# Performance work log

Measured on AMD Instinct MI355X. Metric: run time of the kernel, lower is better.

Reference implementation:

```python
import jax, jax.numpy as jnp
import numpy as np

EPS = 1e-07
B, N, L, K = 256, 512, 4, 1

def setup_inputs() -> dict:
    key = jax.random.key(0)
    k1, k2, k3, k4 = jax.random.split(key, 4)
    x = jax.random.randint(k1, (B, N), 0, L)
    W = jax.random.normal(k2, (N, N), dtype=jnp.float32)
    V_compress = jax.random.normal(k3, (N, L), dtype=jnp.float32)
    E_compress = jax.random.normal(k4, (K, N, N, L, L), dtype=jnp.float32)
    return {"x": x, "W": W, "V_compress": V_compress, "E_compress": E_compress}

def reference(x, W, V_compress, E_compress):
    n = W.shape[0]
    # V: per-variable marginals via softmax over classes
    V = jax.nn.softmax(V_compress, axis=1)                      # (n, l)
    # E: pairwise joints for mixture 0, normalized over (l, l)
    E = jnp.exp(E_compress[0])                                   # (n, n, l, l)
    E = E / E.sum(axis=(-2, -1), keepdims=True)
    A_b = V[:, None, :, None]                                    # row target marginals
    B_b = V[None, :, None, :]                                    # col target marginals
    # IPFP: 2 iterations of row/col marginal rescaling
    for _ in range(2):
        E = E * (A_b / E.sum(axis=3, keepdims=True))
        E = E * (B_b / E.sum(axis=2, keepdims=True))
        E = E / E.sum(axis=(-2, -1), keepdims=True)
    # zero the diagonal blocks and clamp
    E_mask = (1.0 - jnp.eye(n, dtype=E.dtype))[:, :, None, None]
    E = jnp.clip(E * E_mask, 0.0, 1.0)
    # symmetric edge-weight matrix from W
    Ws = jax.nn.sigmoid(W)
    Ws = jnp.tril(Ws, -1)
    Ws = Ws.T + Ws
    L_0 = -Ws + jnp.diag(Ws.sum(axis=1))                         # (n, n)
    # gather per-sample marginals and pairwise joints
    idx = jnp.arange(n)
    Pr = V[idx[None, :], x]                                      # (B, n): Pr[b,i] = V[i, x[b,i]]
    P = E[idx[:, None], idx[None, :], x[:, :, None], x[:, None, :]]  # (B, n, n)
    P = P / (Pr[:, :, None] * Pr[:, None, :])
    WP = Ws[None, :, :] * P                                      # (B, n, n)
    Lap = -WP + jnp.eye(n, dtype=WP.dtype)[None] * WP.sum(axis=2)[:, :, None]
    # matrix-tree: logdet of the (n-1)x(n-1) minor
    _, ld = jnp.linalg.slogdet(Lap[:, 1:, 1:] + EPS)
    _, ld0 = jnp.linalg.slogdet(L_0[1:, 1:] + EPS)
    y = jnp.log(Pr + EPS).sum(axis=1) + ld - ld0                 # (B,)
    return y
```

## Files before the change

### kernel.cpp

```cpp
#include <hip/hip_runtime.h>

#define NN 512
#define NR 511
#define NB 64
#define BATCH 256
#define NMAT 257
#define EPSF 1e-7f

__device__ __forceinline__ float block_reduce_sum_512(float v, float* red) {
#pragma unroll
  for (int off = 32; off > 0; off >>= 1) v += __shfl_down(v, off, 64);
  int tid = threadIdx.x;
  if ((tid & 63) == 0) red[tid >> 6] = v;
  __syncthreads();
  float s = 0.f;
#pragma unroll
  for (int w = 0; w < 8; ++w) s += red[w];
  return s;
}

__global__ void k_softmaxV(const float* __restrict__ Vc, float* __restrict__ V) {
  int i = threadIdx.x;
  float v0 = Vc[i * 4 + 0], v1 = Vc[i * 4 + 1], v2 = Vc[i * 4 + 2], v3 = Vc[i * 4 + 3];
  float mx = fmaxf(fmaxf(v0, v1), fmaxf(v2, v3));
  float e0 = expf(v0 - mx), e1 = expf(v1 - mx), e2 = expf(v2 - mx), e3 = expf(v3 - mx);
  float s = e0 + e1 + e2 + e3;
  V[i * 4 + 0] = e0 / s; V[i * 4 + 1] = e1 / s; V[i * 4 + 2] = e2 / s; V[i * 4 + 3] = e3 / s;
}

__global__ void k_Ws(const float* __restrict__ W, float* __restrict__ Ws) {
  int i = blockIdx.x, j = threadIdx.x;
  float v = 0.f;
  if (i != j) {
    int hi = i > j ? i : j, lo = i > j ? j : i;
    float wv = W[hi * NN + lo];
    v = 1.f / (1.f + expf(-wv));
  }
  Ws[i * NN + j] = v;
}

__global__ void k_E(const float* __restrict__ Ec, const float* __restrict__ V,
                    float* __restrict__ E) {
  int idx = blockIdx.x * blockDim.x + threadIdx.x;
  if (idx >= NN * NN) return;
  int i = idx >> 9, j = idx & 511;
  float e[16];
  const float* src = Ec + (size_t)idx * 16;
#pragma unroll
  for (int t = 0; t < 16; ++t) e[t] = expf(src[t]);
  float tot = 0.f;
#pragma unroll
  for (int t = 0; t < 16; ++t) tot += e[t];
  float rt = 1.f / tot;
#pragma unroll
  for (int t = 0; t < 16; ++t) e[t] *= rt;
  float Vi[4], Vj[4];
#pragma unroll
  for (int a = 0; a < 4; ++a) { Vi[a] = V[i * 4 + a]; Vj[a] = V[j * 4 + a]; }
#pragma unroll
  for (int it = 0; it < 2; ++it) {
#pragma unroll
    for (int a = 0; a < 4; ++a) {
      float rs = e[a * 4 + 0] + e[a * 4 + 1] + e[a * 4 + 2] + e[a * 4 + 3];
      float sc = Vi[a] / rs;
#pragma unroll
      for (int b = 0; b < 4; ++b) e[a * 4 + b] *= sc;
    }
#pragma unroll
    for (int b = 0; b < 4; ++b) {
      float cs = e[0 + b] + e[4 + b] + e[8 + b] + e[12 + b];
      float sc = Vj[b] / cs;
#pragma unroll
      for (int a = 0; a < 4; ++a) e[a * 4 + b] *= sc;
    }
    float t2 = 0.f;
#pragma unroll
    for (int t = 0; t < 16; ++t) t2 += e[t];
    float rt2 = 1.f / t2;
#pragma unroll
    for (int t = 0; t < 16; ++t) e[t] *= rt2;
  }
  float* dst = E + (size_t)idx * 16;
  bool diag = (i == j);
#pragma unroll
  for (int t = 0; t < 16; ++t) {
    float v = diag ? 0.f : e[t];
    dst[t] = fminf(fmaxf(v, 0.f), 1.f);
  }
}

__global__ __launch_bounds__(512)
void k_Pr(const int* __restrict__ x, const float* __restrict__ V,
          float* __restrict__ rPr, float* __restrict__ logPr) {
  __shared__ float red[8];
  int b = blockIdx.x, i = threadIdx.x;
  int xi = x[b * NN + i];
  float pr = V[i * 4 + xi];
  rPr[b * NN + i] = 1.f / pr;
  float s = block_reduce_sum_512(logf(pr + EPSF), red);
  if (i == 0) logPr[b] = s;
}

__global__ __launch_bounds__(512)
void k_build(const int* __restrict__ x, const float* __restrict__ Ws,
             const float* __restrict__ E, const float* __restrict__ rPr,
             float* __restrict__ mats, int m0) {
  int slot = blockIdx.y;
  int m = m0 + slot;
  float* A = mats + (size_t)slot * NN * NN;
  int wv = threadIdx.x >> 6, lane = threadIdx.x & 63;
  int r = blockIdx.x * 8 + wv;
  float* dst = A + (size_t)r * NN + lane * 8;
  if (r == NR) {
    float4 z0 = {0.f, 0.f, 0.f, 0.f};
    float4 z1 = {0.f, 0.f, 0.f, 0.f};
    if (lane == 63) z1.w = 1.f;
    *(float4*)dst = z0;
    *(float4*)(dst + 4) = z1;
    return;
  }
  int i = r + 1;
  int j0 = lane * 8;
  float4 wsa = *(const float4*)&Ws[i * NN + j0];
  float4 wsb = *(const float4*)&Ws[i * NN + j0 + 4];
  float wp[8];
  if (m < BATCH) {
    const int* xm = x + (size_t)m * NN;
    int xi = xm[i];
    int4 xa = *(const int4*)&xm[j0];
    int4 xb = *(const int4*)&xm[j0 + 4];
    const float* rp = rPr + (size_t)m * NN;
    float rpi = rp[i];
    float4 ra = *(const float4*)&rp[j0];
    float4 rb = *(const float4*)&rp[j0 + 4];
    const float* Eb = E + ((((size_t)i << 9) + j0) << 4) + (xi << 2);
    wp[0] = wsa.x * Eb[0 * 16 + xa.x] * (rpi * ra.x);
    wp[1] = wsa.y * Eb[1 * 16 + xa.y] * (rpi * ra.y);
    wp[2] = wsa.z * Eb[2 * 16 + xa.z] * (rpi * ra.z);
    wp[3] = wsa.w * Eb[3 * 16 + xa.w] * (rpi * ra.w);
    wp[4] = wsb.x * Eb[4 * 16 + xb.x] * (rpi * rb.x);
    wp[5] = wsb.y * Eb[5 * 16 + xb.y] * (rpi * rb.y);
    wp[6] = wsb.z * Eb[6 * 16 + xb.z] * (rpi * rb.z);
    wp[7] = wsb.w * Eb[7 * 16 + xb.w] * (rpi * rb.w);
  } else {
    wp[0] = wsa.x; wp[1] = wsa.y; wp[2] = wsa.z; wp[3] = wsa.w;
    wp[4] = wsb.x; wp[5] = wsb.y; wp[6] = wsb.z; wp[7] = wsb.w;
  }
  float rs = ((wp[0] + wp[1]) + (wp[2] + wp[3])) + ((wp[4] + wp[5]) + (wp[6] + wp[7]));
#pragma unroll
  for (int o = 32; o > 0; o >>= 1) rs += __shfl_xor(rs, o, 64);
  float nxt = __shfl_down(wp[0], 1, 64);
  float sh[8] = {wp[1], wp[2], wp[3], wp[4], wp[5], wp[6], wp[7], nxt};
  float out[8];
#pragma unroll
  for (int t = 0; t < 8; ++t) {
    int c = j0 + t;
    float v = -sh[t] + EPSF;
    if (c == r) v += rs;
    if (c == NR) v = 0.f;
    out[t] = v;
  }
  float4 o0 = {out[0], out[1], out[2], out[3]};
  float4 o1 = {out[4], out[5], out[6], out[7]};
  *(float4*)dst = o0;
  *(float4*)(dst + 4) = o1;
}

template <int S>
struct PStepF {
  static __device__ __forceinline__ void run(float (&rr)[64], float (*Prow)[64],
                                             bool own, int tid, float& lgsum) {
    float rinv = 1.f / Prow[S & 1][S];
    if (own && tid > S) {
      float l = rr[S] * rinv;
      rr[S] = l;
      constexpr int C0 = S + 1;
      constexpr int A4 = (C0 + 3) & ~3;
#pragma unroll
      for (int c = C0; c < (A4 < 64 ? A4 : 64); ++c)
        rr[c] = fmaf(-l, Prow[S & 1][c], rr[c]);
#pragma unroll
      for (int g = A4 / 4; g < 16; ++g) {
        float4 u = *(const float4*)&Prow[S & 1][g * 4];
        rr[g * 4 + 0] = fmaf(-l, u.x, rr[g * 4 + 0]);
        rr[g * 4 + 1] = fmaf(-l, u.y, rr[g * 4 + 1]);
        rr[g * 4 + 2] = fmaf(-l, u.z, rr[g * 4 + 2]);
        rr[g * 4 + 3] = fmaf(-l, u.w, rr[g * 4 + 3]);
      }
    }
    if (S + 1 < 64) {
      if (tid == S + 1) {
        lgsum += logf(rr[S + 1]);
#pragma unroll
        for (int c4 = (S + 1) >> 2; c4 < 16; ++c4) {
          float4 v = {rr[c4 * 4 + 0], rr[c4 * 4 + 1], rr[c4 * 4 + 2], rr[c4 * 4 + 3]};
          *(float4*)&Prow[(S + 1) & 1][c4 * 4] = v;
        }
      }
    }
    __syncthreads();
    PStepF<S + 1>::run(rr, Prow, own, tid, lgsum);
  }
};
template <>
struct PStepF<64> {
  static __device__ __forceinline__ void run(float (&)[64], float (*)[64],
                                             bool, int, float&) {}
};

template <int Q>
struct UStep {
  static __device__ __forceinline__ void run(float (&a)[64], const float* L) {
    constexpr int j0 = Q * 4;
    a[j0 + 1] = fmaf(-L[(j0 + 1) * 68 + j0], a[j0], a[j0 + 1]);
    a[j0 + 2] = fmaf(-L[(j0 + 2) * 68 + j0], a[j0], a[j0 + 2]);
    a[j0 + 2] = fmaf(-L[(j0 + 2) * 68 + j0 + 1], a[j0 + 1], a[j0 + 2]);
    a[j0 + 3] = fmaf(-L[(j0 + 3) * 68 + j0], a[j0], a[j0 + 3]);
    a[j0 + 3] = fmaf(-L[(j0 + 3) * 68 + j0 + 1], a[j0 + 1], a[j0 + 3]);
    a[j0 + 3] = fmaf(-L[(j0 + 3) * 68 + j0 + 2], a[j0 + 2], a[j0 + 3]);
#pragma unroll
    for (int t = j0 + 4; t < 64; ++t) {
      float4 Lv = *(const float4*)&L[t * 68 + j0];
      float v = a[t];
      v = fmaf(-Lv.x, a[j0 + 0], v);
      v = fmaf(-Lv.y, a[j0 + 1], v);
      v = fmaf(-Lv.z, a[j0 + 2], v);
      v = fmaf(-Lv.w, a[j0 + 3], v);
      a[t] = v;
    }
    UStep<Q + 1>::run(a, L);
  }
};
template <>
struct UStep<16> {
  static __device__ __forceinline__ void run(float (&)[64], const float*) {}
};

__global__ __launch_bounds__(512)
void k_pu(float* __restrict__ mats, float* __restrict__ ld, int m0, int p) {
  __shared__ __align__(16) float L11[64 * 68];
  __shared__ __align__(16) float Prow[2][64];
  __shared__ float red[8];
  int slot = blockIdx.x;
  float* A = mats + (size_t)slot * NN * NN;
  int tid = threadIdx.x;
  int k0 = p * NB;
  int m = NN - k0;
  int w = m - NB;
  bool own = tid < m;
  float* myrow = A + (size_t)(k0 + tid) * NN + k0;
  float lgsum = 0.f;
  float rr[64];

  if (own) {
#pragma unroll
    for (int c4 = 0; c4 < 16; ++c4) {
      float4 v = *(const float4*)(myrow + c4 * 4);
      rr[c4 * 4 + 0] = v.x; rr[c4 * 4 + 1] = v.y;
      rr[c4 * 4 + 2] = v.z; rr[c4 * 4 + 3] = v.w;
    }
  } else {
#pragma unroll
    for (int c = 0; c < 64; ++c) rr[c] = 0.f;
  }
  if (tid == 0) {
    lgsum += logf(rr[0]);
#pragma unroll
    for (int c4 = 0; c4 < 16; ++c4) {
      float4 v = {rr[c4 * 4 + 0], rr[c4 * 4 + 1], rr[c4 * 4 + 2], rr[c4 * 4 + 3]};
      *(float4*)&Prow[0][c4 * 4] = v;
    }
  }
  __syncthreads();
  PStepF<0>::run(rr, Prow, own, tid, lgsum);
  if (own) {
#pragma unroll
    for (int c4 = 0; c4 < 16; ++c4) {
      float4 v = {rr[c4 * 4 + 0], rr[c4 * 4 + 1], rr[c4 * 4 + 2], rr[c4 * 4 + 3]};
      *(float4*)(myrow + c4 * 4) = v;
    }
  }
  if (tid < 64) {
#pragma unroll
    for (int c4 = 0; c4 < 16; ++c4) {
      float4 v = {rr[c4 * 4 + 0], rr[c4 * 4 + 1], rr[c4 * 4 + 2], rr[c4 * 4 + 3]};
      *(float4*)&L11[tid * 68 + c4 * 4] = v;
    }
  }
  __syncthreads();

  if (w > 0 && tid < w) {
    int col = k0 + NB + tid;
#pragma unroll
    for (int t = 0; t < 64; ++t) rr[t] = A[(size_t)(k0 + t) * NN + col];
    UStep<0>::run(rr, L11);
#pragma unroll
    for (int t = 0; t < 64; ++t) A[(size_t)(k0 + t) * NN + col] = rr[t];
  }

  float s = block_reduce_sum_512(lgsum, red);
  if (tid == 0) {
    int gi = m0 + slot;
    if (p == 0) ld[gi] = s;
    else        ld[gi] += s;
  }
}

__global__ __launch_bounds__(256)
void k_gemm(float* __restrict__ mats, int p) {
  __shared__ __align__(16) float At[64 * 132];
  int k0 = p * NB;
  int w = NN - k0 - NB;
  float* A = mats + (size_t)blockIdx.z * NN * NN;
  int rb = blockIdx.x * 128, cb = blockIdx.y * 128;
  int tid = threadIdx.x;
#pragma unroll
  for (int it = 0; it < 32; ++it) {
    int idx = tid + it * 256;
    int r = idx >> 6, kk = idx & 63;
    int gr = rb + r;
    float v = 0.f;
    if (gr < w) v = A[(size_t)(k0 + NB + gr) * NN + k0 + kk];
    At[kk * 132 + r] = v;
  }
  __syncthreads();
  int ty = tid >> 4, tx = tid & 15;
  int r0 = ty * 8, c0 = tx * 8;
  int gc0 = k0 + NB + cb + c0;
  bool cok = (cb + c0) < w;
  float acc[8][8];
#pragma unroll
  for (int q = 0; q < 8; ++q)
#pragma unroll
    for (int u = 0; u < 8; ++u) acc[q][u] = 0.f;
  float4 bc0 = {0.f, 0.f, 0.f, 0.f}, bc1 = {0.f, 0.f, 0.f, 0.f};
  if (cok) {
    const float* Br = &A[(size_t)k0 * NN + gc0];
    bc0 = *(const float4*)Br;
    bc1 = *(const float4*)(Br + 4);
  }
#pragma unroll 2
  for (int kk = 0; kk < 64; ++kk) {
    float4 bn0 = {0.f, 0.f, 0.f, 0.f}, bn1 = {0.f, 0.f, 0.f, 0.f};
    if (cok && kk < 63) {
      const float* Br = &A[(size_t)(k0 + kk + 1) * NN + gc0];
      bn0 = *(const float4*)Br;
      bn1 = *(const float4*)(Br + 4);
    }
    float4 a0 = *(const float4*)&At[kk * 132 + r0];
    float4 a1 = *(const float4*)&At[kk * 132 + r0 + 4];
    float la[8] = {a0.x, a0.y, a0.z, a0.w, a1.x, a1.y, a1.z, a1.w};
    float lb[8] = {bc0.x, bc0.y, bc0.z, bc0.w, bc1.x, bc1.y, bc1.z, bc1.w};
#pragma unroll
    for (int q = 0; q < 8; ++q)
#pragma unroll
      for (int u = 0; u < 8; ++u) acc[q][u] = fmaf(la[q], lb[u], acc[q][u]);
    bc0 = bn0; bc1 = bn1;
  }
  if (!cok) return;
#pragma unroll
  for (int q = 0; q < 8; ++q) {
    int gr = rb + r0 + q;
    if (gr < w) {
      float* dst = &A[(size_t)(k0 + NB + gr) * NN + gc0];
      float4 v0 = *(const float4*)dst;
      float4 v1 = *(const float4*)(dst + 4);
      v0.x -= acc[q][0]; v0.y -= acc[q][1]; v0.z -= acc[q][2]; v0.w -= acc[q][3];
      v1.x -= acc[q][4]; v1.y -= acc[q][5]; v1.z -= acc[q][6]; v1.w -= acc[q][7];
      *(float4*)dst = v0;
      *(float4*)(dst + 4) = v1;
    }
  }
}

__global__ void k_y(const float* __restrict__ logPr, const float* __restrict__ ld,
                    float* __restrict__ y) {
  int b = threadIdx.x;
  if (b < BATCH) y[b] = logPr[b] + ld[b] - ld[BATCH];
}

extern "C" void kernel_launch(void* const* d_in, const int* in_sizes, int n_in,
                              void* d_out, int out_size, void* d_ws, size_t ws_size,
                              hipStream_t stream) {
  const int* x = (const int*)d_in[0];
  const float* W = (const float*)d_in[1];
  const float* Vc = (const float*)d_in[2];
  const float* Ec = (const float*)d_in[3];
  float* out = (float*)d_out;

  char* ws = (char*)d_ws;
  size_t off = 0;
  auto alloc = [&](size_t bytes) -> void* {
    void* pp = ws + off;
    off = (off + bytes + 255) & ~(size_t)255;
    return pp;
  };
  float* V     = (float*)alloc((size_t)NN * 4 * 4);
  float* Wsbuf = (float*)alloc((size_t)NN * NN * 4);
  float* rPr   = (float*)alloc((size_t)BATCH * NN * 4);
  float* logPr = (float*)alloc((size_t)BATCH * 4);
  float* ld    = (float*)alloc((size_t)NMAT * 4);
  float* E     = (float*)alloc((size_t)NN * NN * 16 * 4);
  size_t per_mat = (size_t)NN * NN * 4;
  size_t remain = ws_size > off ? ws_size - off : 0;
  int cap = (int)(remain / per_mat);
  if (cap > NMAT) cap = NMAT;
  if (cap < 1) cap = 1;
  float* mats = (float*)(ws + off);

  k_softmaxV<<<1, 512, 0, stream>>>(Vc, V);
  k_Ws<<<NN, NN, 0, stream>>>(W, Wsbuf);
  k_E<<<(NN * NN) / 256, 256, 0, stream>>>(Ec, V, E);
  k_Pr<<<BATCH, NN, 0, stream>>>(x, V, rPr, logPr);

  for (int m0 = 0; m0 < NMAT; m0 += cap) {
    int cnt = NMAT - m0 < cap ? NMAT - m0 : cap;
    dim3 gb(64, cnt);
    k_build<<<gb, 512, 0, stream>>>(x, Wsbuf, E, rPr, mats, m0);
    for (int p = 0; p < 8; ++p) {
      k_pu<<<cnt, 512, 0, stream>>>(mats, ld, m0, p);
      int w = NN - p * NB - NB;
      if (w > 0) {
        int nt = (w + 127) / 128;
        dim3 gg(nt, nt, cnt);
        k_gemm<<<gg, 256, 0, stream>>>(mats, p);
      }
    }
  }
  k_y<<<1, 256, 0, stream>>>(logPr, ld, out);
}
```

Before: 1.700 ms.

## Factor diagonal panel in one wavefront and store E plane-major

The 64x64 diagonal block of each panel is now LU-factored by a single wavefront using wave barriers, which replaces the 64 block-wide __syncthreads steps. The remaining panel rows are then eliminated independently from the factored L11 and the stored reciprocal pivots. Separately, the E joint tensor is stored as 16 class-pair planes of NN×NN instead of interleaved 16-float blocks, so gathers in the build kernel use a row-contiguous layout. The cost is serial work concentrated in one wave during the diagonal factorization.

```diff
diff --git a/kernel.cpp b/kernel.cpp
--- a/kernel.cpp
+++ b/kernel.cpp
@@ -6,6 +6,9 @@
 #define BATCH 256
 #define NMAT 257
 #define EPSF 1e-7f
+#define NN2 ((size_t)NN * NN)
+
+#define WSYNC() do { __builtin_amdgcn_wave_barrier(); asm volatile("" ::: "memory"); } while (0)
 
 __device__ __forceinline__ float block_reduce_sum_512(float v, float* red) {
 #pragma unroll
@@ -80,12 +83,11 @@
 #pragma unroll
     for (int t = 0; t < 16; ++t) e[t] *= rt2;
   }
-  float* dst = E + (size_t)idx * 16;
   bool diag = (i == j);
 #pragma unroll
   for (int t = 0; t < 16; ++t) {
     float v = diag ? 0.f : e[t];
-    dst[t] = fminf(fmaxf(v, 0.f), 1.f);
+    E[(size_t)t * NN2 + idx] = fminf(fmaxf(v, 0.f), 1.f);
   }
 }
 
@@ -107,7 +109,7 @@
              float* __restrict__ mats, int m0) {
   int slot = blockIdx.y;
   int m = m0 + slot;
-  float* A = mats + (size_t)slot * NN * NN;
+  float* A = mats + (size_t)slot * NN2;
   int wv = threadIdx.x >> 6, lane = threadIdx.x & 63;
   int r = blockIdx.x * 8 + wv;
   float* dst = A + (size_t)r * NN + lane * 8;
@@ -133,15 +135,15 @@
     float rpi = rp[i];
     float4 ra = *(const float4*)&rp[j0];
     float4 rb = *(const float4*)&rp[j0 + 4];
-    const float* Eb = E + ((((size_t)i << 9) + j0) << 4) + (xi << 2);
-    wp[0] = wsa.x * Eb[0 * 16 + xa.x] * (rpi * ra.x);
-    wp[1] = wsa.y * Eb[1 * 16 + xa.y] * (rpi * ra.y);
-    wp[2] = wsa.z * Eb[2 * 16 + xa.z] * (rpi * ra.z);
-    wp[3] = wsa.w * Eb[3 * 16 + xa.w] * (rpi * ra.w);
-    wp[4] = wsb.x * Eb[4 * 16 + xb.x] * (rpi * rb.x);
-    wp[5] = wsb.y * Eb[5 * 16 + xb.y] * (rpi * rb.y);
-    wp[6] = wsb.z * Eb[6 * 16 + xb.z] * (rpi * rb.z);
-    wp[7] = wsb.w * Eb[7 * 16 + xb.w] * (rpi * rb.w);
+    const float* Eb = E + (size_t)(xi * 4) * NN2 + (size_t)i * NN + j0;
+    wp[0] = wsa.x * Eb[(size_t)xa.x * NN2 + 0] * (rpi * ra.x);
+    wp[1] = wsa.y * Eb[(size_t)xa.y * NN2 + 1] * (rpi * ra.y);
+    wp[2] = wsa.z * Eb[(size_t)xa.z * NN2 + 2] * (rpi * ra.z);
+    wp[3] = wsa.w * Eb[(size_t)xa.w * NN2 + 3] * (rpi * ra.w);
+    wp[4] = wsb.x * Eb[(size_t)xb.x * NN2 + 4] * (rpi * rb.x);
+    wp[5] = wsb.y * Eb[(size_t)xb.y * NN2 + 5] * (rpi * rb.y);
+    wp[6] = wsb.z * Eb[(size_t)xb.z * NN2 + 6] * (rpi * rb.z);
+    wp[7] = wsb.w * Eb[(size_t)xb.w * NN2 + 7] * (rpi * rb.w);
   } else {
     wp[0] = wsa.x; wp[1] = wsa.y; wp[2] = wsa.z; wp[3] = wsa.w;
     wp[4] = wsb.x; wp[5] = wsb.y; wp[6] = wsb.z; wp[7] = wsb.w;
@@ -167,21 +169,21 @@
 }
 
 template <int S>
-struct PStepF {
-  static __device__ __forceinline__ void run(float (&rr)[64], float (*Prow)[64],
-                                             bool own, int tid, float& lgsum) {
-    float rinv = 1.f / Prow[S & 1][S];
-    if (own && tid > S) {
+struct WStepL {
+  static __device__ __forceinline__ void run(float (&rr)[64], float* L11f,
+                                             float* RinvL, int lane, float& lgsum) {
+    float rinv = RinvL[S];
+    if (lane > S) {
       float l = rr[S] * rinv;
       rr[S] = l;
       constexpr int C0 = S + 1;
       constexpr int A4 = (C0 + 3) & ~3;
 #pragma unroll
       for (int c = C0; c < (A4 < 64 ? A4 : 64); ++c)
-        rr[c] = fmaf(-l, Prow[S & 1][c], rr[c]);
+        rr[c] = fmaf(-l, L11f[S * 68 + c], rr[c]);
 #pragma unroll
       for (int g = A4 / 4; g < 16; ++g) {
-        float4 u = *(const float4*)&Prow[S & 1][g * 4];
+        float4 u = *(const float4*)&L11f[S * 68 + g * 4];
         rr[g * 4 + 0] = fmaf(-l, u.x, rr[g * 4 + 0]);
         rr[g * 4 + 1] = fmaf(-l, u.y, rr[g * 4 + 1]);
         rr[g * 4 + 2] = fmaf(-l, u.z, rr[g * 4 + 2]);
@@ -189,23 +191,52 @@
       }
     }
     if (S + 1 < 64) {
-      if (tid == S + 1) {
+      if (lane == S + 1) {
         lgsum += logf(rr[S + 1]);
-#pragma unroll
-        for (int c4 = (S + 1) >> 2; c4 < 16; ++c4) {
+        RinvL[S + 1] = 1.f / rr[S + 1];
+#pragma unroll
+        for (int c4 = 0; c4 < 16; ++c4) {
           float4 v = {rr[c4 * 4 + 0], rr[c4 * 4 + 1], rr[c4 * 4 + 2], rr[c4 * 4 + 3]};
-          *(float4*)&Prow[(S + 1) & 1][c4 * 4] = v;
+          *(float4*)&L11f[(S + 1) * 68 + c4 * 4] = v;
         }
       }
     }
-    __syncthreads();
-    PStepF<S + 1>::run(rr, Prow, own, tid, lgsum);
+    WSYNC();
+    WStepL<S + 1>::run(rr, L11f, RinvL, lane, lgsum);
   }
 };
 template <>
-struct PStepF<64> {
-  static __device__ __forceinline__ void run(float (&)[64], float (*)[64],
-                                             bool, int, float&) {}
+struct WStepL<64> {
+  static __device__ __forceinline__ void run(float (&)[64], float*, float*,
+                                             int, float&) {}
+};
+
+template <int S>
+struct BStep {
+  static __device__ __forceinline__ void run(float (&a)[64], const float* L,
+                                             const float* Rinv) {
+    float l = a[S] * Rinv[S];
+    a[S] = l;
+    constexpr int c0 = S + 1;
+    constexpr int ca = (c0 + 3) & ~3;
+#pragma unroll
+    for (int c = c0; c < (ca < 64 ? ca : 64); ++c)
+      a[c] = fmaf(-l, L[S * 68 + c], a[c]);
+#pragma unroll
+    for (int c4 = ca / 4; c4 < 16; ++c4) {
+      float4 u = *(const float4*)&L[S * 68 + c4 * 4];
+      a[c4 * 4 + 0] = fmaf(-l, u.x, a[c4 * 4 + 0]);
+      a[c4 * 4 + 1] = fmaf(-l, u.y, a[c4 * 4 + 1]);
+      a[c4 * 4 + 2] = fmaf(-l, u.z, a[c4 * 4 + 2]);
+      a[c4 * 4 + 3] = fmaf(-l, u.w, a[c4 * 4 + 3]);
+    }
+    BStep<S + 1>::run(a, L, Rinv);
+  }
+};
+template <>
+struct BStep<64> {
+  static __device__ __forceinline__ void run(float (&)[64], const float*,
+                                             const float*) {}
 };
 
 template <int Q>
@@ -239,10 +270,10 @@
 __global__ __launch_bounds__(512)
 void k_pu(float* __restrict__ mats, float* __restrict__ ld, int m0, int p) {
   __shared__ __align__(16) float L11[64 * 68];
-  __shared__ __align__(16) float Prow[2][64];
+  __shared__ float RinvL[64];
   __shared__ float red[8];
   int slot = blockIdx.x;
-  float* A = mats + (size_t)slot * NN * NN;
+  float* A = mats + (size_t)slot * NN2;
   int tid = threadIdx.x;
   int k0 = p * NB;
   int m = NN - k0;
@@ -263,31 +294,36 @@
 #pragma unroll
     for (int c = 0; c < 64; ++c) rr[c] = 0.f;
   }
-  if (tid == 0) {
-    lgsum += logf(rr[0]);
-#pragma unroll
-    for (int c4 = 0; c4 < 16; ++c4) {
-      float4 v = {rr[c4 * 4 + 0], rr[c4 * 4 + 1], rr[c4 * 4 + 2], rr[c4 * 4 + 3]};
-      *(float4*)&Prow[0][c4 * 4] = v;
-    }
+
+  if (tid < 64) {
+    if (tid == 0) {
+      lgsum += logf(rr[0]);
+      RinvL[0] = 1.f / rr[0];
+#pragma unroll
+      for (int c4 = 0; c4 < 16; ++c4) {
+        float4 v = {rr[c4 * 4 + 0], rr[c4 * 4 + 1], rr[c4 * 4 + 2], rr[c4 * 4 + 3]};
+        *(float4*)&L11[c4 * 4] = v;
+      }
+    }
+    WSYNC();
+    WStepL<0>::run(rr, L11, RinvL, tid, lgsum);
   }
   __syncthreads();
-  PStepF<0>::run(rr, Prow, own, tid, lgsum);
-  if (own) {
+
+  if (tid < 64) {
 #pragma unroll
     for (int c4 = 0; c4 < 16; ++c4) {
       float4 v = {rr[c4 * 4 + 0], rr[c4 * 4 + 1], rr[c4 * 4 + 2], rr[c4 * 4 + 3]};
       *(float4*)(myrow + c4 * 4) = v;
     }
-  }
-  if (tid < 64) {
+  } else if (own) {
+    BStep<0>::run(rr, L11, RinvL);
 #pragma unroll
     for (int c4 = 0; c4 < 16; ++c4) {
       float4 v = {rr[c4 * 4 + 0], rr[c4 * 4 + 1], rr[c4 * 4 + 2], rr[c4 * 4 + 3]};
-      *(float4*)&L11[tid * 68 + c4 * 4] = v;
-    }
-  }
-  __syncthreads();
+      *(float4*)(myrow + c4 * 4) = v;
+    }
+  }
 
   if (w > 0 && tid < w) {
     int col = k0 + NB + tid;
@@ -311,7 +347,7 @@
   __shared__ __align__(16) float At[64 * 132];
   int k0 = p * NB;
   int w = NN - k0 - NB;
-  float* A = mats + (size_t)blockIdx.z * NN * NN;
+  float* A = mats + (size_t)blockIdx.z * NN2;
   int rb = blockIdx.x * 128, cb = blockIdx.y * 128;
   int tid = threadIdx.x;
 #pragma unroll
@@ -396,12 +432,12 @@
     return pp;
   };
   float* V     = (float*)alloc((size_t)NN * 4 * 4);
-  float* Wsbuf = (float*)alloc((size_t)NN * NN * 4);
+  float* Wsbuf = (float*)alloc(NN2 * 4);
   float* rPr   = (float*)alloc((size_t)BATCH * NN * 4);
   float* logPr = (float*)alloc((size_t)BATCH * 4);
   float* ld    = (float*)alloc((size_t)NMAT * 4);
-  float* E     = (float*)alloc((size_t)NN * NN * 16 * 4);
-  size_t per_mat = (size_t)NN * NN * 4;
+  float* E     = (float*)alloc(NN2 * 16 * 4);
+  size_t per_mat = NN2 * 4;
   size_t remain = ws_size > off ? ws_size - off : 0;
   int cap = (int)(remain / per_mat);
   if (cap > NMAT) cap = NMAT;
```

After: 1.843 ms. +8.4%, slower.
